# Kernel optimization log

Measured on AMD Instinct MI355X. Metric: run time of the kernel, lower is better.

## Reference

```python
import jax, jax.numpy as jnp
import numpy as np

B, N, K, IN_C, OUT_C = 8, 20000, 9, 64, 64


def setup_inputs() -> dict:
    key = jax.random.key(0)
    k1, k2, k3, k4, k5, k6 = jax.random.split(key, 6)
    x = jax.random.normal(k1, (B, N, IN_C), dtype=jnp.float32)
    neighbor_index = jax.random.randint(k2, (B, N, K), 0, N, dtype=jnp.int64)
    # adjweight initialized to identity per original code (eye expanded over num_pts)
    adjweight = jnp.broadcast_to(jnp.eye(K, dtype=jnp.float32), (N, K, K))
    # conv: Linear(in_c*K -> out_c); mlp_out: Linear(in_c -> out_c)
    conv_w = jax.random.normal(k3, (OUT_C, IN_C * K), dtype=jnp.float32) / np.sqrt(IN_C * K)
    conv_b = jax.random.normal(k4, (OUT_C,), dtype=jnp.float32) * 0.01
    mlp_w = jax.random.normal(k5, (OUT_C, IN_C), dtype=jnp.float32) / np.sqrt(IN_C)
    mlp_b = jax.random.normal(k6, (OUT_C,), dtype=jnp.float32) * 0.01
    return {"x": x, "neighbor_index": neighbor_index, "adjweight": adjweight,
            "conv_w": conv_w, "conv_b": conv_b, "mlp_w": mlp_w, "mlp_b": mlp_b}


def reference(x, neighbor_index, adjweight, conv_w, conv_b, mlp_w, mlp_b):
    bsize, num_pts, feats = x.shape
    num_neighbor = neighbor_index.shape[-1]
    # zero_padding mask: last point zeroed
    mask = jnp.ones((1, num_pts, 1), dtype=x.dtype).at[0, -1, 0].set(0.0)
    x = x * mask
    # per-batch gather of neighbor features: [B, N, K, F]
    x_neighbors = jax.vmap(lambda xb, ib: xb[ib])(x, neighbor_index)
    # learnable per-point KxK mixing over the neighbor dim: bnkf,nkt->bntf
    x_neighbors = jnp.einsum('bnkf,nkt->bntf', x_neighbors, adjweight)
    x_neighbors = jax.nn.elu(x_neighbors).reshape(bsize, num_pts, num_neighbor * feats)
    out_feat = jax.nn.elu(x_neighbors @ conv_w.T + conv_b) * mask
    x_res = x @ mlp_w.T + mlp_b
    return out_feat + x_res
```

## Files before the change

### kernel.cpp

```cpp
#include <hip/hip_runtime.h>

#define BB 8
#define NN 20000
#define KK 9
#define CC 64
#define KC 576
#define ROWS (BB*NN)

#define WST_ELE   (18*64*32)
#define WST2_ELE  (2*64*32)
#define ADJ_ELE   (NN*88)
#define WST_OFF   0
#define WST2_OFF  (WST_ELE)
#define ADJ_OFF   (WST_ELE + WST2_ELE)
#define ZERO_EOFF (ADJ_OFF + ADJ_ELE)
#define PREP_THREADS (ADJ_ELE)

typedef __bf16 bf16x8 __attribute__((ext_vector_type(8)));
typedef float  f32x4  __attribute__((ext_vector_type(4)));
typedef unsigned short u16x8 __attribute__((ext_vector_type(8)));

__device__ __forceinline__ unsigned short f2bf(float f) {
    unsigned u = __builtin_bit_cast(unsigned, f);
    u += 0x7FFFu + ((u >> 16) & 1u);
    return (unsigned short)(u >> 16);
}
__device__ __forceinline__ float bfhi2f(unsigned w) {
    return __builtin_bit_cast(float, w & 0xFFFF0000u);
}
__device__ __forceinline__ float bflo2f(unsigned w) {
    return __builtin_bit_cast(float, w << 16);
}
__device__ __forceinline__ float elu_f(float v) {
    return v > 0.0f ? v : (__expf(v) - 1.0f);
}

__global__ void __launch_bounds__(256) paiconv_prep(
        const float* __restrict__ adj,
        const float* __restrict__ conv_w,
        const float* __restrict__ mlp_w,
        unsigned short* __restrict__ ws16) {
    int tid = blockIdx.x * 256 + threadIdx.x;

    if (tid < WST_ELE) {
        int kk = tid & 31, o = (tid >> 5) & 63, mch = tid >> 11;
        int c = mch / 9, t = mch - 9 * c;
        ws16[WST_OFF + tid] = f2bf(conv_w[o * KC + t * 64 + c * 32 + kk]);
    }
    if (tid < WST2_ELE) {
        int kk = tid & 31, o = (tid >> 5) & 63, c2 = tid >> 11;
        ws16[WST2_OFF + tid] = f2bf(mlp_w[o * 64 + c2 * 32 + kk]);
    }
    if (tid < 128) {
        ((unsigned short*)(ws16 + ZERO_EOFF))[tid] = 0;
    }
    if (tid < ADJ_ELE) {
        int n = tid / 88, j = tid - 88 * n;
        ws16[ADJ_OFF + tid] = (j < 81) ? f2bf(adj[n * 81 + j]) : (unsigned short)0;
    }
}

__global__ void __launch_bounds__(256, 2) paiconv_main(
        const float* __restrict__ x,
        const int*   __restrict__ nidx,
        const float* __restrict__ conv_b,
        const float* __restrict__ mlp_b,
        const unsigned short* __restrict__ ws16,
        float* __restrict__ out) {
    const int tx   = threadIdx.x;
    const int lane = tx & 63;
    const int l15  = lane & 15;
    const int q    = lane >> 4;
    const int wave = __builtin_amdgcn_readfirstlane(tx >> 6);
    const int rowbase = blockIdx.x * 64 + wave * 16;
    const int b   = rowbase / NN;
    const int n0  = rowbase - b * NN;
    const int myrow = rowbase + l15;
    const int myn   = n0 + l15;

    const unsigned short* Wst  = ws16 + WST_OFF;
    const unsigned short* Wst2 = ws16 + WST2_OFF;
    const unsigned short* Adj  = ws16 + ADJ_OFF;
    const float* Z = (const float*)(ws16 + ZERO_EOFF);

    const float* bp[KK];
    #pragma unroll
    for (int k = 0; k < KK; ++k) {
        int idx = nidx[myrow * KK + k];
        const float* p = x + (size_t)(b * NN + idx) * 64;
        bp[k] = (idx == NN - 1) ? Z : p;
    }

    unsigned adjw[44];
    {
        const uint4* ap = (const uint4*)(Adj + (size_t)myn * 88);
        #pragma unroll
        for (int u = 0; u < 11; ++u) {
            uint4 w = ap[u];
            adjw[4 * u + 0] = w.x; adjw[4 * u + 1] = w.y;
            adjw[4 * u + 2] = w.z; adjw[4 * u + 3] = w.w;
        }
    }

    f32x4 acc[4];
    f32x4 acc2[4];
    #pragma unroll
    for (int ot = 0; ot < 4; ++ot) { acc[ot] = (f32x4)0.0f; acc2[ot] = (f32x4)0.0f; }

    #pragma unroll 1
    for (int c = 0; c < 2; ++c) {
        float v[KK][8];
        #pragma unroll
        for (int k = 0; k < KK; ++k) {
            const float* p = bp[k] + c * 32 + q * 8;
            f32x4 lo = *(const f32x4*)p;
            f32x4 hi = *(const f32x4*)(p + 4);
            #pragma unroll
            for (int i = 0; i < 4; ++i) { v[k][i] = lo[i]; v[k][4 + i] = hi[i]; }
        }
        #pragma unroll
        for (int t = 0; t < KK; ++t) {
            float m[8] = {0.f,0.f,0.f,0.f,0.f,0.f,0.f,0.f};
            #pragma unroll
            for (int k = 0; k < KK; ++k) {
                const int j = k * 9 + t;
                unsigned w = adjw[j >> 1];
                float a = (j & 1) ? bfhi2f(w) : bflo2f(w);
                #pragma unroll
                for (int i = 0; i < 8; ++i) m[i] = __builtin_fmaf(a, v[k][i], m[i]);
            }
            u16x8 pk;
            #pragma unroll
            for (int i = 0; i < 8; ++i) pk[i] = f2bf(elu_f(m[i]));
            bf16x8 afrag = __builtin_bit_cast(bf16x8, pk);
            const int mch = c * 9 + t;
            #pragma unroll
            for (int ot = 0; ot < 4; ++ot) {
                const u16x8* wp = (const u16x8*)(Wst + mch * 2048 + (ot * 16 + l15) * 32 + q * 8);
                bf16x8 bfrag = __builtin_bit_cast(bf16x8, *wp);
                acc[ot] = __builtin_amdgcn_mfma_f32_16x16x32_bf16(afrag, bfrag, acc[ot], 0, 0, 0);
            }
        }
    }

    #pragma unroll
    for (int c2 = 0; c2 < 2; ++c2) {
        const float* ps = x + (size_t)myrow * 64 + c2 * 32 + q * 8;
        f32x4 lo = *(const f32x4*)ps;
        f32x4 hi = *(const f32x4*)(ps + 4);
        const bool dead = (myn == NN - 1);
        u16x8 pk;
        #pragma unroll
        for (int i = 0; i < 8; ++i) {
            float xv = (i < 4) ? lo[i] : hi[i - 4];
            pk[i] = f2bf(dead ? 0.0f : xv);
        }
        bf16x8 a2 = __builtin_bit_cast(bf16x8, pk);
        #pragma unroll
        for (int ot = 0; ot < 4; ++ot) {
            const u16x8* wp = (const u16x8*)(Wst2 + c2 * 2048 + (ot * 16 + l15) * 32 + q * 8);
            bf16x8 b2 = __builtin_bit_cast(bf16x8, *wp);
            acc2[ot] = __builtin_amdgcn_mfma_f32_16x16x32_bf16(a2, b2, acc2[ot], 0, 0, 0);
        }
    }

    #pragma unroll
    for (int ot = 0; ot < 4; ++ot) {
        const int o = ot * 16 + l15;
        const float cb = conv_b[o];
        const float mb = mlp_b[o];
        #pragma unroll
        for (int i = 0; i < 4; ++i) {
            const int rr = 4 * q + i;
            const int nrow = n0 + rr;
            float f = elu_f(acc[ot][i] + cb);
            if (nrow == NN - 1) f = 0.0f;
            f += acc2[ot][i] + mb;
            out[(size_t)(rowbase + rr) * 64 + o] = f;
        }
    }
}

extern "C" void kernel_launch(void* const* d_in, const int* in_sizes, int n_in,
                              void* d_out, int out_size, void* d_ws, size_t ws_size,
                              hipStream_t stream) {
    const float* x      = (const float*)d_in[0];
    const int*   nidx   = (const int*)  d_in[1];
    const float* adj    = (const float*)d_in[2];
    const float* conv_w = (const float*)d_in[3];
    const float* conv_b = (const float*)d_in[4];
    const float* mlp_w  = (const float*)d_in[5];
    const float* mlp_b  = (const float*)d_in[6];
    unsigned short* ws16 = (unsigned short*)d_ws;
    float* out = (float*)d_out;

    const int prep_blocks = (PREP_THREADS + 255) / 256;
    paiconv_prep<<<prep_blocks, 256, 0, stream>>>(adj, conv_w, mlp_w, ws16);

    const int main_blocks = ROWS / 64;
    paiconv_main<<<main_blocks, 256, 0, stream>>>(x, nidx, conv_b, mlp_b, ws16, out);
}
```

Measured before the change: 305.7 us.

## Pre-convert x to bf16 in prep and gather bf16 neighbors; stage output stores

The prep kernel now converts the whole x tensor to bf16, with the masked last point zeroed, and packs the adjacency weights with 8-wide vector stores. The main kernel gathers neighbor rows from this bf16 copy, which halves the gather bytes and drops the pointer-select masking. Blocks are interleaved across batches, presumably for L2 locality. Output goes through LDS so each row is written with coalesced float4 nontemporal stores, and index and adjacency loads are marked nontemporal. The cost is an extra full pass over x in prep (read fp32, write bf16) and extra workspace.

After: 302.8 us. No clear change (-1.0%).

```diff
diff --git a/kernel.cpp b/kernel.cpp
--- a/kernel.cpp
+++ b/kernel.cpp
@@ -3,100 +3,118 @@
 #define BB 8
 #define NN 20000
 #define KK 9
-#define CC 64
 #define KC 576
 #define ROWS (BB*NN)
 
-#define WST_ELE   (18*64*32)
-#define WST2_ELE  (2*64*32)
+#define WST_ELE   36864
+#define WST2_ELE  4096
 #define ADJ_ELE   (NN*88)
+#define XB_ELE    (ROWS*64)
 #define WST_OFF   0
-#define WST2_OFF  (WST_ELE)
-#define ADJ_OFF   (WST_ELE + WST2_ELE)
-#define ZERO_EOFF (ADJ_OFF + ADJ_ELE)
-#define PREP_THREADS (ADJ_ELE)
+#define WST2_OFF  36864
+#define ADJ_OFF   40960
+#define XB_OFF    (ADJ_OFF + ADJ_ELE)
 
 typedef __bf16 bf16x8 __attribute__((ext_vector_type(8)));
 typedef float  f32x4  __attribute__((ext_vector_type(4)));
 typedef unsigned short u16x8 __attribute__((ext_vector_type(8)));
+typedef unsigned u32x4 __attribute__((ext_vector_type(4)));
 
 __device__ __forceinline__ unsigned short f2bf(float f) {
     unsigned u = __builtin_bit_cast(unsigned, f);
     u += 0x7FFFu + ((u >> 16) & 1u);
     return (unsigned short)(u >> 16);
 }
-__device__ __forceinline__ float bfhi2f(unsigned w) {
-    return __builtin_bit_cast(float, w & 0xFFFF0000u);
-}
-__device__ __forceinline__ float bflo2f(unsigned w) {
-    return __builtin_bit_cast(float, w << 16);
-}
-__device__ __forceinline__ float elu_f(float v) {
-    return v > 0.0f ? v : (__expf(v) - 1.0f);
-}
+__device__ __forceinline__ float bfhi2f(unsigned w) { return __builtin_bit_cast(float, w & 0xFFFF0000u); }
+__device__ __forceinline__ float bflo2f(unsigned w) { return __builtin_bit_cast(float, w << 16); }
+__device__ __forceinline__ float elu_f(float v) { return v > 0.0f ? v : (__expf(v) - 1.0f); }
 
 __global__ void __launch_bounds__(256) paiconv_prep(
+        const float* __restrict__ x,
         const float* __restrict__ adj,
         const float* __restrict__ conv_w,
         const float* __restrict__ mlp_w,
         unsigned short* __restrict__ ws16) {
-    int tid = blockIdx.x * 256 + threadIdx.x;
-
+    const int tid = blockIdx.x * 256 + threadIdx.x;
+
+    if (tid < XB_ELE / 8) {
+        const int e = tid * 8;
+        const int r = e >> 6;
+        const int n = r % NN;
+        u16x8 pk;
+        if (n == NN - 1) {
+            #pragma unroll
+            for (int i = 0; i < 8; ++i) pk[i] = 0;
+        } else {
+            f32x4 lo = *(const f32x4*)(x + e);
+            f32x4 hi = *(const f32x4*)(x + e + 4);
+            #pragma unroll
+            for (int i = 0; i < 4; ++i) { pk[i] = f2bf(lo[i]); pk[4 + i] = f2bf(hi[i]); }
+        }
+        *(u16x8*)(ws16 + XB_OFF + e) = pk;
+    }
+    if (tid < NN * 11) {
+        const int n = tid / 11;
+        const int j = (tid - n * 11) * 8;
+        u16x8 pk;
+        #pragma unroll
+        for (int m = 0; m < 8; ++m) {
+            const int jj = j + m;
+            pk[m] = (jj < 81) ? f2bf(adj[n * 81 + jj]) : (unsigned short)0;
+        }
+        *(u16x8*)(ws16 + ADJ_OFF + n * 88 + j) = pk;
+    }
     if (tid < WST_ELE) {
-        int kk = tid & 31, o = (tid >> 5) & 63, mch = tid >> 11;
-        int c = mch / 9, t = mch - 9 * c;
+        const int kk = tid & 31, o = (tid >> 5) & 63, mch = tid >> 11;
+        const int c = mch / 9, t = mch - 9 * c;
         ws16[WST_OFF + tid] = f2bf(conv_w[o * KC + t * 64 + c * 32 + kk]);
     }
     if (tid < WST2_ELE) {
-        int kk = tid & 31, o = (tid >> 5) & 63, c2 = tid >> 11;
+        const int kk = tid & 31, o = (tid >> 5) & 63, c2 = tid >> 11;
         ws16[WST2_OFF + tid] = f2bf(mlp_w[o * 64 + c2 * 32 + kk]);
     }
-    if (tid < 128) {
-        ((unsigned short*)(ws16 + ZERO_EOFF))[tid] = 0;
-    }
-    if (tid < ADJ_ELE) {
-        int n = tid / 88, j = tid - 88 * n;
-        ws16[ADJ_OFF + tid] = (j < 81) ? f2bf(adj[n * 81 + j]) : (unsigned short)0;
-    }
 }
 
 __global__ void __launch_bounds__(256, 2) paiconv_main(
-        const float* __restrict__ x,
         const int*   __restrict__ nidx,
         const float* __restrict__ conv_b,
         const float* __restrict__ mlp_b,
         const unsigned short* __restrict__ ws16,
         float* __restrict__ out) {
+    __shared__ float sm[4][16][68];
+
     const int tx   = threadIdx.x;
     const int lane = tx & 63;
     const int l15  = lane & 15;
     const int q    = lane >> 4;
-    const int wave = __builtin_amdgcn_readfirstlane(tx >> 6);
-    const int rowbase = blockIdx.x * 64 + wave * 16;
-    const int b   = rowbase / NN;
-    const int n0  = rowbase - b * NN;
-    const int myrow = rowbase + l15;
-    const int myn   = n0 + l15;
+    const int wave = tx >> 6;
+    const int batch = blockIdx.x & 7;
+    const int chunk = blockIdx.x >> 3;
+    const int n0    = chunk * 64 + wave * 16;
+    if (n0 >= NN) return;
+    const int rowbase = batch * NN + n0;
+    const int myrow   = rowbase + l15;
+    const int myn     = n0 + l15;
 
     const unsigned short* Wst  = ws16 + WST_OFF;
     const unsigned short* Wst2 = ws16 + WST2_OFF;
     const unsigned short* Adj  = ws16 + ADJ_OFF;
-    const float* Z = (const float*)(ws16 + ZERO_EOFF);
-
-    const float* bp[KK];
+    const unsigned short* XB   = ws16 + XB_OFF;
+    const unsigned short* XBb  = XB + (size_t)batch * NN * 64;
+
+    int voff[KK];
     #pragma unroll
     for (int k = 0; k < KK; ++k) {
-        int idx = nidx[myrow * KK + k];
-        const float* p = x + (size_t)(b * NN + idx) * 64;
-        bp[k] = (idx == NN - 1) ? Z : p;
+        const int idx = __builtin_nontemporal_load(nidx + myrow * KK + k);
+        voff[k] = idx * 64 + q * 8;
     }
 
     unsigned adjw[44];
     {
-        const uint4* ap = (const uint4*)(Adj + (size_t)myn * 88);
+        const u32x4* ap = (const u32x4*)(Adj + (size_t)myn * 88);
         #pragma unroll
         for (int u = 0; u < 11; ++u) {
-            uint4 w = ap[u];
+            u32x4 w = __builtin_nontemporal_load(ap + u);
             adjw[4 * u + 0] = w.x; adjw[4 * u + 1] = w.y;
             adjw[4 * u + 2] = w.z; adjw[4 * u + 3] = w.w;
         }
@@ -112,11 +130,12 @@
         float v[KK][8];
         #pragma unroll
         for (int k = 0; k < KK; ++k) {
-            const float* p = bp[k] + c * 32 + q * 8;
-            f32x4 lo = *(const f32x4*)p;
-            f32x4 hi = *(const f32x4*)(p + 4);
-            #pragma unroll
-            for (int i = 0; i < 4; ++i) { v[k][i] = lo[i]; v[k][4 + i] = hi[i]; }
+            u16x8 pv = *(const u16x8*)(XBb + voff[k] + c * 32);
+            u32x4 pw = __builtin_bit_cast(u32x4, pv);
+            v[k][0] = bflo2f(pw.x); v[k][1] = bfhi2f(pw.x);
+            v[k][2] = bflo2f(pw.y); v[k][3] = bfhi2f(pw.y);
+            v[k][4] = bflo2f(pw.z); v[k][5] = bfhi2f(pw.z);
+            v[k][6] = bflo2f(pw.w); v[k][7] = bfhi2f(pw.w);
         }
         #pragma unroll
         for (int t = 0; t < KK; ++t) {
@@ -145,17 +164,7 @@
 
     #pragma unroll
     for (int c2 = 0; c2 < 2; ++c2) {
-        const float* ps = x + (size_t)myrow * 64 + c2 * 32 + q * 8;
-        f32x4 lo = *(const f32x4*)ps;
-        f32x4 hi = *(const f32x4*)(ps + 4);
-        const bool dead = (myn == NN - 1);
-        u16x8 pk;
-        #pragma unroll
-        for (int i = 0; i < 8; ++i) {
-            float xv = (i < 4) ? lo[i] : hi[i - 4];
-            pk[i] = f2bf(dead ? 0.0f : xv);
-        }
-        bf16x8 a2 = __builtin_bit_cast(bf16x8, pk);
+        bf16x8 a2 = *(const bf16x8*)(XB + (size_t)myrow * 64 + c2 * 32 + q * 8);
         #pragma unroll
         for (int ot = 0; ot < 4; ++ot) {
             const u16x8* wp = (const u16x8*)(Wst2 + c2 * 2048 + (ot * 16 + l15) * 32 + q * 8);
@@ -172,12 +181,17 @@
         #pragma unroll
         for (int i = 0; i < 4; ++i) {
             const int rr = 4 * q + i;
-            const int nrow = n0 + rr;
             float f = elu_f(acc[ot][i] + cb);
-            if (nrow == NN - 1) f = 0.0f;
+            if (n0 + rr == NN - 1) f = 0.0f;
             f += acc2[ot][i] + mb;
-            out[(size_t)(rowbase + rr) * 64 + o] = f;
-        }
+            sm[wave][rr][o] = f;
+        }
+    }
+    #pragma unroll
+    for (int p = 0; p < 4; ++p) {
+        const int r = p * 4 + q;
+        f32x4 vv = *(const f32x4*)&sm[wave][r][l15 * 4];
+        __builtin_nontemporal_store(vv, (f32x4*)(out + (size_t)(rowbase + r) * 64 + l15 * 4));
     }
 }
 
@@ -194,9 +208,9 @@
     unsigned short* ws16 = (unsigned short*)d_ws;
     float* out = (float*)d_out;
 
-    const int prep_blocks = (PREP_THREADS + 255) / 256;
-    paiconv_prep<<<prep_blocks, 256, 0, stream>>>(adj, conv_w, mlp_w, ws16);
-
-    const int main_blocks = ROWS / 64;
-    paiconv_main<<<main_blocks, 256, 0, stream>>>(x, nidx, conv_b, mlp_b, ws16, out);
-}
+    const int prep_blocks = (XB_ELE / 8) / 256;
+    paiconv_prep<<<prep_blocks, 256, 0, stream>>>(x, adj, conv_w, mlp_w, ws16);
+
+    const int main_blocks = 8 * 313;
+    paiconv_main<<<main_blocks, 256, 0, stream>>>(nidx, conv_b, mlp_b, ws16, out);
+}
```
